# Kernel optimization log

Measured on AMD Instinct MI355X. Metric: run time of the kernel, lower is better.

Reference implementation:

```python
import jax, jax.numpy as jnp
import numpy as np

BETA = 0.05
ALPHA = 0.01
CROSSCAM_EPOCH = 5
BG_KNN = 50
C, L, D = 8, 4096, 2048   # cameras, pseudo-classes per camera, feature dim
B = 256                   # batch, cam-sorted blocks of PERCAM samples
PERCAM = B // C


def setup_inputs() -> dict:
    key = jax.random.key(0)
    kf, km = jax.random.split(key)
    features = jax.random.normal(kf, (B, D), dtype=jnp.float32)
    # cams sorted in blocks; per-camera targets unique (PK-sampler style), spread over [0, L)
    cams = jnp.repeat(jnp.arange(C, dtype=jnp.int32), PERCAM)
    targets = jnp.tile(jnp.arange(PERCAM, dtype=jnp.int32) * (L // PERCAM), C)
    # dataset-level arrays: every camera observes all L labels -> identity class mapper,
    # concate_intra_class == tile(arange(L), C)
    all_img_cams = jnp.repeat(jnp.arange(C, dtype=jnp.int32), L)
    all_pseudo_label = jnp.tile(jnp.arange(L, dtype=jnp.int32), C)
    mem = jax.random.normal(km, (C, L, D), dtype=jnp.float32)
    init_intra_id_feat = mem / jnp.linalg.norm(mem, axis=-1, keepdims=True)
    return {"features": features, "targets": targets, "cams": cams,
            "all_pseudo_label": all_pseudo_label, "all_img_cams": all_img_cams,
            "init_intra_id_feat": init_intra_id_feat, "epoch": 10, "batch_ind": 0}


def _forward(features, init_intra_id_feat, targets, cams, epoch):
    Cn, Ln, Dn = init_intra_id_feat.shape
    Bn = features.shape[0]
    percam = Bn // Cn
    mem0 = jax.lax.stop_gradient(init_intra_id_feat)  # proxy memory buffer (detached in torch)
    # --- EMA memory update (torch.no_grad); (cam, target) pairs unique in batch ---
    f_sg = jax.lax.stop_gradient(features)
    old = mem0[cams, targets]                                   # [B, D] gather
    new = ALPHA * old + (1.0 - ALPHA) * f_sg
    new = new / jnp.linalg.norm(new, axis=1, keepdims=True)
    mem = mem0.at[cams, targets].set(new)                       # scatter update
    # --- per-camera proxy cross-entropy (cams are sorted blocks of `percam`) ---
    fn = features / jnp.linalg.norm(features, axis=1, keepdims=True)
    memn = mem / jnp.linalg.norm(mem, axis=-1, keepdims=True)   # rows already unit; faithful
    logits = jnp.einsum('cbd,cld->cbl', fn.reshape(Cn, percam, Dn), memn) / BETA
    lsm = jax.nn.log_softmax(logits, axis=-1)
    t = targets.reshape(Cn, percam)
    ce = -jnp.take_along_axis(lsm, t[..., None], axis=-1)[..., 0]   # [C, percam]
    loss = ce.mean(axis=1).sum()   # torch sums per-camera mean CE over unique batch cams
    # --- cross-camera associative loss (all_cam_feats built from pre-update memory) ---
    if epoch >= CROSSCAM_EPOCH:
        allf = mem0.reshape(Cn * Ln, Dn)
        allf = allf / jnp.linalg.norm(allf, axis=1, keepdims=True)
        sims = fn @ allf.T                                      # [B, C*L]
        # ori_asso_ind: label t appears once per camera block in concate_intra_class
        pos = targets[:, None] + jnp.arange(Cn)[None, :] * Ln   # [B, C]
        rows = jnp.arange(Bn)[:, None]
        pos_logits = sims[rows, pos] / BETA                     # [B, C]
        masked = sims.at[rows, pos].set(-10000.0)               # temp_sims masking
        topv, _ = jax.lax.top_k(masked, BG_KNN)                 # hardest negatives
        cat = jnp.concatenate([pos_logits, topv / BETA], axis=1)  # [B, C+BG_KNN]
        ls2 = jax.nn.log_softmax(cat, axis=1)
        per = -ls2[:, :Cn].sum(axis=1) / Cn                     # soft target 1/|ori| on positives
        loss = loss + 0.5 * per.reshape(Cn, percam).mean(axis=1).sum()
    return loss.reshape(1)


def reference(features, targets, cams, all_pseudo_label, all_img_cams,
              init_intra_id_feat, epoch, batch_ind):
    # all_pseudo_label / all_img_cams determine concate_intra_class; by construction
    # each camera holds all L labels, so positive indices are computed analytically.
    return _forward(features, init_intra_id_feat, targets, cams, epoch)
```

## Files before the change

### kernel.cpp

```cpp
#include <hip/hip_runtime.h>
#include <hip/hip_bf16.h>


#define Dn 2048
#define Ln 4096
#define Cn 8
#define Bn 256
#define NTOT 32768
#define INVB 20.0f
#define KNN 50

typedef __attribute__((ext_vector_type(8))) short short8;
typedef __attribute__((ext_vector_type(4))) float f32x4;

__device__ __forceinline__ unsigned short f2b(float f) {
    unsigned u = __float_as_uint(f);
    unsigned r = (u + 0x7FFFu + ((u >> 16) & 1u)) >> 16;
    return (unsigned short)r;
}

__device__ __forceinline__ unsigned pack2(float x, float y) {
    __hip_bfloat162 h = __float22bfloat162_rn(float2{x, y});
    unsigned u; __builtin_memcpy(&u, &h, 4); return u;
}

__global__ __launch_bounds__(256) void prep_kernel(
    const float* __restrict__ feat, const float* __restrict__ mem0,
    const int* __restrict__ targets, const int* __restrict__ cams,
    float* __restrict__ fn, float* __restrict__ nrows,
    unsigned short* __restrict__ fnb) {
    int i = blockIdx.x, tid = threadIdx.x;
    int c = cams[i], t = targets[i];
    const float* f = feat + (size_t)i * Dn;
    const float* o = mem0 + ((size_t)c * Ln + t) * Dn;
    float fv[8], nv[8];
    float s1 = 0.f, s2 = 0.f;
#pragma unroll
    for (int r = 0; r < 8; ++r) {
        int idx = tid + (r << 8);
        float a = f[idx], bb = o[idx];
        float n = 0.99f * a + 0.01f * bb;
        fv[r] = a; nv[r] = n;
        s1 += a * a; s2 += n * n;
    }
    __shared__ float red[2][4];
    for (int off = 32; off > 0; off >>= 1) {
        s1 += __shfl_down(s1, off);
        s2 += __shfl_down(s2, off);
    }
    int wv = tid >> 6;
    if ((tid & 63) == 0) { red[0][wv] = s1; red[1][wv] = s2; }
    __syncthreads();
    s1 = red[0][0] + red[0][1] + red[0][2] + red[0][3];
    s2 = red[1][0] + red[1][1] + red[1][2] + red[1][3];
    float r1 = 1.0f / sqrtf(s1), r2 = 1.0f / sqrtf(s2);
#pragma unroll
    for (int r = 0; r < 8; ++r) {
        int idx = tid + (r << 8);
        float a = fv[r] * r1;
        fn[(size_t)i * Dn + idx] = a;
        fnb[(size_t)i * Dn + idx] = f2b(a);
        nrows[(size_t)i * Dn + idx] = nv[r] * r2;
    }
}

#define GSTEP(KIT, CUR, NXT)                                                      \
  {                                                                               \
    if ((KIT) + 1 < 32) {                                                         \
      _Pragma("unroll") for (int mf = 0; mf < 4; ++mf)                            \
        _Pragma("unroll") for (int kb = 0; kb < 2; ++kb)                          \
          av[NXT][mf][kb] =                                                       \
            *(const short8*)&fnb[aoff[mf] + ((KIT) + 1) * 64 + kb * 32];          \
    }                                                                             \
    if ((KIT) + 2 < 32) {                                                         \
      _Pragma("unroll") for (int r = 0; r < 4; ++r)                               \
        rb[CUR][r] = *(const float4*)&mem0[boff[r] + ((KIT) + 2) * 64];           \
    }                                                                             \
    _Pragma("unroll") for (int kb = 0; kb < 2; ++kb) {                            \
      short8 bv[4];                                                               \
      _Pragma("unroll") for (int nf = 0; nf < 4; ++nf)                            \
        bv[nf] = *(const short8*)&lB[CUR][(nf * 16 + fr) * 72 + kb * 32 + fg * 8];\
      _Pragma("unroll") for (int mf = 0; mf < 4; ++mf)                            \
        _Pragma("unroll") for (int nf = 0; nf < 4; ++nf)                          \
          acc[mf][nf] = __builtin_amdgcn_mfma_f32_16x16x32_bf16(                  \
              av[CUR][mf][kb], bv[nf], acc[mf][nf], 0, 0, 0);                     \
    }                                                                             \
    if ((KIT) + 1 < 32) {                                                         \
      _Pragma("unroll") for (int r = 0; r < 4; ++r) {                             \
        float4 v = rb[NXT][r];                                                    \
        uint2 h; h.x = pack2(v.x, v.y); h.y = pack2(v.z, v.w);                    \
        *(uint2*)&lB[NXT][(r * 16 + btr) * 72 + btc * 4] = h;                     \
      }                                                                           \
    }                                                                             \
    __syncthreads();                                                              \
  }

__global__ __launch_bounds__(256, 2) void gemm_sims(
    const float* __restrict__ mem0, const unsigned short* __restrict__ fnb,
    float* __restrict__ sims) {
    __shared__ __align__(16) unsigned short lB[2][64 * 72];
    int tid = threadIdx.x;
    int n0 = blockIdx.x * 64;
    int lane = tid & 63, wv = tid >> 6;
    int fr = lane & 15, fg = lane >> 4;
    int btr = tid >> 4, btc = tid & 15;

    f32x4 acc[4][4];
#pragma unroll
    for (int a = 0; a < 4; ++a)
#pragma unroll
        for (int b = 0; b < 4; ++b)
#pragma unroll
            for (int k = 0; k < 4; ++k) acc[a][b][k] = 0.0f;

    size_t aoff[4], boff[4];
#pragma unroll
    for (int mf = 0; mf < 4; ++mf)
        aoff[mf] = (size_t)(wv * 64 + mf * 16 + fr) * Dn + fg * 8;
#pragma unroll
    for (int r = 0; r < 4; ++r)
        boff[r] = (size_t)(n0 + r * 16 + btr) * Dn + btc * 4;

    float4 rb[2][4];
    short8 av[2][4][2];
#pragma unroll
    for (int r = 0; r < 4; ++r) rb[0][r] = *(const float4*)&mem0[boff[r]];
#pragma unroll
    for (int r = 0; r < 4; ++r) rb[1][r] = *(const float4*)&mem0[boff[r] + 64];
#pragma unroll
    for (int mf = 0; mf < 4; ++mf)
#pragma unroll
        for (int kb = 0; kb < 2; ++kb)
            av[0][mf][kb] = *(const short8*)&fnb[aoff[mf] + kb * 32];
#pragma unroll
    for (int r = 0; r < 4; ++r) {
        float4 v = rb[0][r];
        uint2 h; h.x = pack2(v.x, v.y); h.y = pack2(v.z, v.w);
        *(uint2*)&lB[0][(r * 16 + btr) * 72 + btc * 4] = h;
    }
    __syncthreads();

    for (int k2 = 0; k2 < 16; ++k2) {
        GSTEP(2 * k2, 0, 1);
        GSTEP(2 * k2 + 1, 1, 0);
    }

    float* tbuf = (float*)lB;
    int row16 = lane & 15, seg = lane >> 4;
#pragma unroll
    for (int mf = 0; mf < 4; ++mf) {
#pragma unroll
        for (int nf = 0; nf < 4; ++nf)
#pragma unroll
            for (int r = 0; r < 4; ++r)
                tbuf[wv * 1088 + (fg * 4 + r) * 68 + nf * 16 + fr] = acc[mf][nf][r];
        __syncthreads();
#pragma unroll
        for (int q = 0; q < 4; ++q) {
            float4 v = *(float4*)&tbuf[wv * 1088 + row16 * 68 + seg * 16 + q * 4];
            int m = wv * 64 + mf * 16 + row16;
            *(float4*)&sims[(size_t)m * NTOT + n0 + seg * 16 + q * 4] = v;
        }
        __syncthreads();
    }
}

__global__ __launch_bounds__(256) void dots_kernel(
    const float* __restrict__ fn, const float* __restrict__ nrows,
    float* __restrict__ sdot_all) {
    int i = blockIdx.x, tid = threadIdx.x;
    int lane = tid & 63, wv = tid >> 6;
    int c = i >> 5;
    float f[32];
    const float* frp = fn + (size_t)i * Dn;
#pragma unroll
    for (int r = 0; r < 32; ++r) f[r] = frp[lane + (r << 6)];
    for (int jj = 0; jj < 8; ++jj) {
        int j = wv * 8 + jj;
        const float* nr = nrows + (size_t)(c * 32 + j) * Dn;
        float d = 0.f;
#pragma unroll
        for (int r = 0; r < 32; ++r) d += f[r] * nr[lane + (r << 6)];
        for (int o = 32; o > 0; o >>= 1) d += __shfl_down(d, o);
        if (lane == 0) sdot_all[i * 32 + j] = d;
    }
}

__global__ __launch_bounds__(256) void fused_kernel(
    const float* __restrict__ sims, const float* __restrict__ sdot_all,
    const int* __restrict__ targets, float* __restrict__ out) {
    __shared__ int hist[4][1024];
    __shared__ int ghist[64];
    __shared__ float buf[512];
    __shared__ int cnt, sh_bstar, sh_r, sh_total;
    __shared__ float wred[4], wmax4[4], wmin4[4], cesum[4];
    int i = blockIdx.x, tid = threadIdx.x;
    int wv = tid >> 6, lane = tid & 63;
    int t = targets[i], c = i >> 5, b = i & 31;
    const float* row = sims + (size_t)i * NTOT;

    float mx = -3e38f, mn = 3e38f, ce_p = 0.f;
    for (int q = 0; q < 128; ++q) {
        int j = tid + (q << 8);
        float v = row[j];
        if ((j >> 12) == c) ce_p += expf(v * INVB);
        if ((j & (Ln - 1)) != t) { mx = fmaxf(mx, v); mn = fminf(mn, v); }
    }
    for (int o = 32; o > 0; o >>= 1) {
        ce_p += __shfl_down(ce_p, o);
        mx = fmaxf(mx, __shfl_down(mx, o));
        mn = fminf(mn, __shfl_down(mn, o));
    }
    if (lane == 0) { cesum[wv] = ce_p; wmax4[wv] = mx; wmin4[wv] = mn; }
    __syncthreads();
    float hi = fmaxf(fmaxf(wmax4[0], wmax4[1]), fmaxf(wmax4[2], wmax4[3]));
    float lo = fminf(fminf(wmin4[0], wmin4[1]), fminf(wmin4[2], wmin4[3]));
    float rng = fmaxf(hi - lo, 1e-30f);

    float thr = 0.f, scale = 0.f;
    for (int att = 0; att < 3; ++att) {
        float frac = (att == 0) ? 0.25f : ((att == 1) ? 0.5f : 1.0001f);
        thr = hi - rng * frac;
        scale = 1023.0f / fmaxf(hi - thr, 1e-30f);
        for (int k = tid; k < 4096; k += 256) ((int*)hist)[k] = 0;
        __syncthreads();
        for (int q = 0; q < 128; ++q) {
            int j = tid + (q << 8);
            float v = row[j];
            if (v > thr && (j & (Ln - 1)) != t) {
                int bin = min(1023, (int)((v - thr) * scale));
                atomicAdd(&hist[wv][bin], 1);
            }
        }
        __syncthreads();
        for (int k = tid; k < 1024; k += 256)
            hist[0][k] = hist[0][k] + hist[1][k] + hist[2][k] + hist[3][k];
        __syncthreads();
        if (tid < 64) {
            int s = 0;
#pragma unroll
            for (int k = 0; k < 16; ++k) s += hist[0][tid * 16 + k];
            ghist[tid] = s;
        }
        __syncthreads();
        if (tid == 0) {
            int total = 0;
            for (int g = 0; g < 64; ++g) total += ghist[g];
            sh_total = total;
            if (total >= KNN) {
                int cum = 0, g = 63;
                for (; g > 0; --g) { if (cum + ghist[g] >= KNN) break; cum += ghist[g]; }
                int bb = g * 16 + 15;
                for (;; --bb) { int h = hist[0][bb]; if (cum + h >= KNN) break; cum += h; }
                sh_bstar = bb;
                sh_r = KNN - cum;
            }
        }
        __syncthreads();
        if (sh_total >= KNN) break;
        __syncthreads();
    }
    int bstar = sh_bstar;
    if (tid == 0) cnt = 0;
    __syncthreads();
    float lsum = 0.f;
    for (int q = 0; q < 128; ++q) {
        int j = tid + (q << 8);
        float v = row[j];
        if (v <= thr || (j & (Ln - 1)) == t) continue;
        int bin = min(1023, (int)((v - thr) * scale));
        if (bin > bstar) {
            lsum += expf(v * INVB);
        } else if (bin == bstar) {
            int p = atomicAdd(&cnt, 1);
            if (p < 512) buf[p] = v;
        }
    }
    for (int o = 32; o > 0; o >>= 1) lsum += __shfl_down(lsum, o);
    if (lane == 0) wred[wv] = lsum;
    __syncthreads();
    if (wv == 0) {
        int nb = min(cnt, 512);
        int r = sh_r;
        float bsum = 0.f;
        for (int s = 0; s < r; ++s) {
            float mv = -3e38f; int mi = 0;
            for (int k = lane; k < nb; k += 64) {
                float v = buf[k];
                if (v > mv) { mv = v; mi = k; }
            }
            for (int o = 32; o > 0; o >>= 1) {
                float ov = __shfl_down(mv, o);
                int oi = __shfl_down(mi, o);
                if (ov > mv) { mv = ov; mi = oi; }
            }
            mi = __shfl(mi, 0); mv = __shfl(mv, 0);
            if (lane == 0) { buf[mi] = -3e38f; bsum += expf(mv * INVB); }
            __builtin_amdgcn_wave_barrier();
        }
        if (lane == 0) {
            float S = wred[0] + wred[1] + wred[2] + wred[3] + bsum;
            float psum = 0.f, pls = 0.f;
#pragma unroll
            for (int c2 = 0; c2 < Cn; ++c2) {
                float pv = row[t + c2 * Ln] * INVB;
                psum += expf(pv);
                pls += pv;
            }
            S += psum;
            float per = logf(S) - pls * (1.0f / Cn);
            float sd = sdot_all[i * 32 + b];
            float Sce = cesum[0] + cesum[1] + cesum[2] + cesum[3]
                        - expf(row[(c << 12) + t] * INVB) + expf(sd * INVB);
            float ce = logf(Sce) - sd * INVB;
            atomicAdd(out, ce * (1.0f / 32.0f) + 0.5f * per * (1.0f / 32.0f));
        }
    }
}

extern "C" void kernel_launch(void* const* d_in, const int* in_sizes, int n_in,
                              void* d_out, int out_size, void* d_ws, size_t ws_size,
                              hipStream_t stream) {
    const float* feat    = (const float*)d_in[0];
    const int*   targets = (const int*)d_in[1];
    const int*   cams    = (const int*)d_in[2];
    const float* mem0    = (const float*)d_in[5];
    float* out = (float*)d_out;
    char* ws = (char*)d_ws;
    float*          fn    = (float*)(ws);
    float*          nrows = (float*)(ws + (size_t)(2 << 20));
    unsigned short* fnb   = (unsigned short*)(ws + (size_t)(4 << 20));
    float*          sdot  = (float*)(ws + (size_t)(6 << 20));
    float*          sims  = (float*)(ws + (size_t)(8 << 20));

    hipMemsetAsync(d_out, 0, (size_t)out_size * sizeof(float), stream);
    prep_kernel<<<Bn, 256, 0, stream>>>(feat, mem0, targets, cams, fn, nrows, fnb);
    gemm_sims<<<NTOT / 64, 256, 0, stream>>>(mem0, fnb, sims);
    dots_kernel<<<Bn, 256, 0, stream>>>(fn, nrows, sdot);
    fused_kernel<<<Bn, 256, 0, stream>>>(sims, sdot, targets, out);
}
```

Before: 506.1 us.

## Replace histogram top-k with bisection threshold and fold dot kernel into fused pass

Removes the separate dots_kernel and computes only the one needed diagonal dot (sample vs its own updated memory row) inside the fused kernel, since only sdot[i*32+b] was ever used. The histogram-based top-50 selection is replaced by a bisection on a threshold that counts candidates per pass, followed by collecting all candidates above the threshold into a 4096-entry LDS buffer and doing 50 wave-wide argmax passes. Row reads are vectorised to float4. Bisection may take up to 12 full passes over the 128 KB row, and the final 50 selection steps scan up to 4096 entries, which could cost more than the old single-bin refinement.

Result: slower. 542.7 us (+7.2%).

```diff
diff --git a/kernel.cpp b/kernel.cpp
--- a/kernel.cpp
+++ b/kernel.cpp
@@ -9,6 +9,7 @@
 #define NTOT 32768
 #define INVB 20.0f
 #define KNN 50
+#define BUFCAP 4096
 
 typedef __attribute__((ext_vector_type(8))) short short8;
 typedef __attribute__((ext_vector_type(4))) float f32x4;
@@ -165,127 +166,94 @@
     }
 }
 
-__global__ __launch_bounds__(256) void dots_kernel(
-    const float* __restrict__ fn, const float* __restrict__ nrows,
-    float* __restrict__ sdot_all) {
-    int i = blockIdx.x, tid = threadIdx.x;
-    int lane = tid & 63, wv = tid >> 6;
-    int c = i >> 5;
-    float f[32];
-    const float* frp = fn + (size_t)i * Dn;
-#pragma unroll
-    for (int r = 0; r < 32; ++r) f[r] = frp[lane + (r << 6)];
-    for (int jj = 0; jj < 8; ++jj) {
-        int j = wv * 8 + jj;
-        const float* nr = nrows + (size_t)(c * 32 + j) * Dn;
-        float d = 0.f;
-#pragma unroll
-        for (int r = 0; r < 32; ++r) d += f[r] * nr[lane + (r << 6)];
-        for (int o = 32; o > 0; o >>= 1) d += __shfl_down(d, o);
-        if (lane == 0) sdot_all[i * 32 + j] = d;
-    }
-}
-
 __global__ __launch_bounds__(256) void fused_kernel(
-    const float* __restrict__ sims, const float* __restrict__ sdot_all,
-    const int* __restrict__ targets, float* __restrict__ out) {
-    __shared__ int hist[4][1024];
-    __shared__ int ghist[64];
-    __shared__ float buf[512];
-    __shared__ int cnt, sh_bstar, sh_r, sh_total;
-    __shared__ float wred[4], wmax4[4], wmin4[4], cesum[4];
+    const float* __restrict__ sims, const float* __restrict__ fn,
+    const float* __restrict__ nrows, const int* __restrict__ targets,
+    float* __restrict__ out) {
+    __shared__ float buf[BUFCAP];
+    __shared__ float fred[4][4];
+    __shared__ int   ired[4];
+    __shared__ int   s_cnt;
+    __shared__ float s_sd;
     int i = blockIdx.x, tid = threadIdx.x;
     int wv = tid >> 6, lane = tid & 63;
-    int t = targets[i], c = i >> 5, b = i & 31;
+    int t = targets[i], c = i >> 5;
     const float* row = sims + (size_t)i * NTOT;
 
-    float mx = -3e38f, mn = 3e38f, ce_p = 0.f;
-    for (int q = 0; q < 128; ++q) {
-        int j = tid + (q << 8);
-        float v = row[j];
-        if ((j >> 12) == c) ce_p += expf(v * INVB);
-        if ((j & (Ln - 1)) != t) { mx = fmaxf(mx, v); mn = fminf(mn, v); }
+    {
+        const float* fp = fn + (size_t)i * Dn;
+        const float* np_ = nrows + (size_t)i * Dn;
+        float d = 0.f;
+#pragma unroll
+        for (int r = 0; r < 8; ++r) { int k = tid + (r << 8); d += fp[k] * np_[k]; }
+        for (int o = 32; o > 0; o >>= 1) d += __shfl_down(d, o);
+        if (lane == 0) fred[0][wv] = d;
+    }
+    float mx = -3e38f, mn = 3e38f, ce = 0.f;
+    for (int q = 0; q < 32; ++q) {
+        int j4 = (tid + (q << 8)) << 2;
+        float4 v = *(const float4*)&row[j4];
+        if ((j4 >> 12) == c)
+            ce += expf(v.x * INVB) + expf(v.y * INVB) + expf(v.z * INVB) + expf(v.w * INVB);
+        int jm = j4 & (Ln - 1);
+        if (jm + 0 != t) { mx = fmaxf(mx, v.x); mn = fminf(mn, v.x); }
+        if (jm + 1 != t) { mx = fmaxf(mx, v.y); mn = fminf(mn, v.y); }
+        if (jm + 2 != t) { mx = fmaxf(mx, v.z); mn = fminf(mn, v.z); }
+        if (jm + 3 != t) { mx = fmaxf(mx, v.w); mn = fminf(mn, v.w); }
     }
     for (int o = 32; o > 0; o >>= 1) {
-        ce_p += __shfl_down(ce_p, o);
         mx = fmaxf(mx, __shfl_down(mx, o));
         mn = fminf(mn, __shfl_down(mn, o));
-    }
-    if (lane == 0) { cesum[wv] = ce_p; wmax4[wv] = mx; wmin4[wv] = mn; }
-    __syncthreads();
-    float hi = fmaxf(fmaxf(wmax4[0], wmax4[1]), fmaxf(wmax4[2], wmax4[3]));
-    float lo = fminf(fminf(wmin4[0], wmin4[1]), fminf(wmin4[2], wmin4[3]));
+        ce += __shfl_down(ce, o);
+    }
+    if (lane == 0) { fred[1][wv] = mx; fred[2][wv] = mn; fred[3][wv] = ce; }
+    __syncthreads();
+    float hi = fmaxf(fmaxf(fred[1][0], fred[1][1]), fmaxf(fred[1][2], fred[1][3]));
+    float lo = fminf(fminf(fred[2][0], fred[2][1]), fminf(fred[2][2], fred[2][3]));
+    float cesum = fred[3][0] + fred[3][1] + fred[3][2] + fred[3][3];
+    float sd = fred[0][0] + fred[0][1] + fred[0][2] + fred[0][3];
     float rng = fmaxf(hi - lo, 1e-30f);
 
-    float thr = 0.f, scale = 0.f;
-    for (int att = 0; att < 3; ++att) {
-        float frac = (att == 0) ? 0.25f : ((att == 1) ? 0.5f : 1.0001f);
-        thr = hi - rng * frac;
-        scale = 1023.0f / fmaxf(hi - thr, 1e-30f);
-        for (int k = tid; k < 4096; k += 256) ((int*)hist)[k] = 0;
+    float tL = lo - 1e-6f * rng, tH = hi;
+    float thr = hi - 0.25f * rng;
+    for (int it = 0; it < 12; ++it) {
+        int cnt = 0;
+        for (int q = 0; q < 32; ++q) {
+            int j4 = (tid + (q << 8)) << 2;
+            float4 v = *(const float4*)&row[j4];
+            int jm = j4 & (Ln - 1);
+            cnt += (v.x > thr && jm + 0 != t);
+            cnt += (v.y > thr && jm + 1 != t);
+            cnt += (v.z > thr && jm + 2 != t);
+            cnt += (v.w > thr && jm + 3 != t);
+        }
+        for (int o = 32; o > 0; o >>= 1) cnt += __shfl_down(cnt, o);
+        if (lane == 0) ired[wv] = cnt;
         __syncthreads();
-        for (int q = 0; q < 128; ++q) {
-            int j = tid + (q << 8);
-            float v = row[j];
-            if (v > thr && (j & (Ln - 1)) != t) {
-                int bin = min(1023, (int)((v - thr) * scale));
-                atomicAdd(&hist[wv][bin], 1);
-            }
-        }
+        int total = ired[0] + ired[1] + ired[2] + ired[3];
+        if (total >= KNN && total <= BUFCAP) break;
+        if (total < KNN) tH = thr; else tL = thr;
+        thr = 0.5f * (tL + tH);
         __syncthreads();
-        for (int k = tid; k < 1024; k += 256)
-            hist[0][k] = hist[0][k] + hist[1][k] + hist[2][k] + hist[3][k];
-        __syncthreads();
-        if (tid < 64) {
-            int s = 0;
-#pragma unroll
-            for (int k = 0; k < 16; ++k) s += hist[0][tid * 16 + k];
-            ghist[tid] = s;
-        }
-        __syncthreads();
-        if (tid == 0) {
-            int total = 0;
-            for (int g = 0; g < 64; ++g) total += ghist[g];
-            sh_total = total;
-            if (total >= KNN) {
-                int cum = 0, g = 63;
-                for (; g > 0; --g) { if (cum + ghist[g] >= KNN) break; cum += ghist[g]; }
-                int bb = g * 16 + 15;
-                for (;; --bb) { int h = hist[0][bb]; if (cum + h >= KNN) break; cum += h; }
-                sh_bstar = bb;
-                sh_r = KNN - cum;
-            }
-        }
-        __syncthreads();
-        if (sh_total >= KNN) break;
-        __syncthreads();
-    }
-    int bstar = sh_bstar;
-    if (tid == 0) cnt = 0;
-    __syncthreads();
-    float lsum = 0.f;
-    for (int q = 0; q < 128; ++q) {
-        int j = tid + (q << 8);
-        float v = row[j];
-        if (v <= thr || (j & (Ln - 1)) == t) continue;
-        int bin = min(1023, (int)((v - thr) * scale));
-        if (bin > bstar) {
-            lsum += expf(v * INVB);
-        } else if (bin == bstar) {
-            int p = atomicAdd(&cnt, 1);
-            if (p < 512) buf[p] = v;
-        }
-    }
-    for (int o = 32; o > 0; o >>= 1) lsum += __shfl_down(lsum, o);
-    if (lane == 0) wred[wv] = lsum;
+    }
+    if (tid == 0) s_cnt = 0;
+    __syncthreads();
+    for (int q = 0; q < 32; ++q) {
+        int j4 = (tid + (q << 8)) << 2;
+        float4 v = *(const float4*)&row[j4];
+        int jm = j4 & (Ln - 1);
+        if (v.x > thr && jm + 0 != t) { int p = atomicAdd(&s_cnt, 1); if (p < BUFCAP) buf[p] = v.x; }
+        if (v.y > thr && jm + 1 != t) { int p = atomicAdd(&s_cnt, 1); if (p < BUFCAP) buf[p] = v.y; }
+        if (v.z > thr && jm + 2 != t) { int p = atomicAdd(&s_cnt, 1); if (p < BUFCAP) buf[p] = v.z; }
+        if (v.w > thr && jm + 3 != t) { int p = atomicAdd(&s_cnt, 1); if (p < BUFCAP) buf[p] = v.w; }
+    }
     __syncthreads();
     if (wv == 0) {
-        int nb = min(cnt, 512);
-        int r = sh_r;
-        float bsum = 0.f;
-        for (int s = 0; s < r; ++s) {
+        int nc = min(s_cnt, BUFCAP);
+        float tsum = 0.f;
+        for (int s = 0; s < KNN; ++s) {
             float mv = -3e38f; int mi = 0;
-            for (int k = lane; k < nb; k += 64) {
+            for (int k = lane; k < nc; k += 64) {
                 float v = buf[k];
                 if (v > mv) { mv = v; mi = k; }
             }
@@ -295,11 +263,10 @@
                 if (ov > mv) { mv = ov; mi = oi; }
             }
             mi = __shfl(mi, 0); mv = __shfl(mv, 0);
-            if (lane == 0) { buf[mi] = -3e38f; bsum += expf(mv * INVB); }
+            if (lane == 0) { buf[mi] = -3e38f; tsum += expf(mv * INVB); }
             __builtin_amdgcn_wave_barrier();
         }
         if (lane == 0) {
-            float S = wred[0] + wred[1] + wred[2] + wred[3] + bsum;
             float psum = 0.f, pls = 0.f;
 #pragma unroll
             for (int c2 = 0; c2 < Cn; ++c2) {
@@ -307,13 +274,11 @@
                 psum += expf(pv);
                 pls += pv;
             }
-            S += psum;
+            float S = tsum + psum;
             float per = logf(S) - pls * (1.0f / Cn);
-            float sd = sdot_all[i * 32 + b];
-            float Sce = cesum[0] + cesum[1] + cesum[2] + cesum[3]
-                        - expf(row[(c << 12) + t] * INVB) + expf(sd * INVB);
-            float ce = logf(Sce) - sd * INVB;
-            atomicAdd(out, ce * (1.0f / 32.0f) + 0.5f * per * (1.0f / 32.0f));
+            float Sce = cesum - expf(row[(c << 12) + t] * INVB) + expf(sd * INVB);
+            float ceL = logf(Sce) - sd * INVB;
+            atomicAdd(out, ceL * (1.0f / 32.0f) + 0.5f * per * (1.0f / 32.0f));
         }
     }
 }
@@ -330,12 +295,10 @@
     float*          fn    = (float*)(ws);
     float*          nrows = (float*)(ws + (size_t)(2 << 20));
     unsigned short* fnb   = (unsigned short*)(ws + (size_t)(4 << 20));
-    float*          sdot  = (float*)(ws + (size_t)(6 << 20));
     float*          sims  = (float*)(ws + (size_t)(8 << 20));
 
     hipMemsetAsync(d_out, 0, (size_t)out_size * sizeof(float), stream);
     prep_kernel<<<Bn, 256, 0, stream>>>(feat, mem0, targets, cams, fn, nrows, fnb);
     gemm_sims<<<NTOT / 64, 256, 0, stream>>>(mem0, fnb, sims);
-    dots_kernel<<<Bn, 256, 0, stream>>>(fn, nrows, sdot);
-    fused_kernel<<<Bn, 256, 0, stream>>>(sims, sdot, targets, out);
-}
+    fused_kernel<<<Bn, 256, 0, stream>>>(sims, fn, nrows, targets, out);
+}
```
